# Optimization experiments

Hardware: AMD Instinct MI355X
Metric: run time of the kernel (lower is better)

Reference implementation:

```python
import jax, jax.numpy as jnp
import numpy as np

D_MODEL = 1024
N_HEAD = 16
D_HEAD = D_MODEL // N_HEAD


def setup_inputs() -> dict:
    key = jax.random.key(0)
    ks = jax.random.split(key, 6)
    B, T = 2, 2048
    scale = 1.0 / np.sqrt(D_MODEL)
    return {
        "x_q": jax.random.normal(ks[0], (B, T, D_MODEL), dtype=jnp.float32),
        "x_kv": jax.random.normal(ks[1], (B, T, D_MODEL), dtype=jnp.float32),
        "w_q": jax.random.normal(ks[2], (D_MODEL, D_MODEL), dtype=jnp.float32) * scale,
        "w_k": jax.random.normal(ks[3], (D_MODEL, D_MODEL), dtype=jnp.float32) * scale,
        "w_v": jax.random.normal(ks[4], (D_MODEL, D_MODEL), dtype=jnp.float32) * scale,
        "w_o": jax.random.normal(ks[5], (D_MODEL, D_MODEL), dtype=jnp.float32) * scale,
    }


def reference(x_q, x_kv, w_q, w_k, w_v, w_o):
    B, Tq, C = x_q.shape
    Tk = x_kv.shape[1]
    # torch Linear: y = x @ W.T  (W is [out, in])
    q = (x_q @ w_q.T).reshape(B, Tq, N_HEAD, D_HEAD).transpose(0, 2, 1, 3)
    k = (x_kv @ w_k.T).reshape(B, Tk, N_HEAD, D_HEAD).transpose(0, 2, 1, 3)
    v = (x_kv @ w_v.T).reshape(B, Tk, N_HEAD, D_HEAD).transpose(0, 2, 1, 3)
    scores = jnp.einsum('bhqd,bhkd->bhqk', q, k) / jnp.sqrt(jnp.float32(D_HEAD))
    attn = jax.nn.softmax(scores, axis=-1)  # [B, H, Tq, Tk]
    out = jnp.einsum('bhqk,bhkd->bhqd', attn, v)
    out = out.transpose(0, 2, 1, 3).reshape(B, Tq, C)
    out = out @ w_o.T
    return (out, attn)
```

## Files before the change

### kernel.cpp

```cpp
#include <hip/hip_runtime.h>
#include <stdint.h>
#include <type_traits>

typedef unsigned short u16;
typedef __attribute__((ext_vector_type(8))) short bf16x8;
typedef __attribute__((ext_vector_type(4))) float f32x4;
typedef __attribute__((ext_vector_type(4))) int   i32x4;

#define TSEQ   2048
#define DMODEL 1024
#define NHEAD  16
#define DHEAD  64
#define SCALE2 0.18033688011112042f

__device__ __forceinline__ u16 f2bf(float f) {
  union { float f; uint32_t u; } v; v.f = f;
  uint32_t r = v.u + 0x7FFFu + ((v.u >> 16) & 1u);
  return (u16)(r >> 16);
}

__device__ __forceinline__ float bf2f(uint32_t bits) {
  union { uint32_t u; float f; } v; v.u = bits << 16;
  return v.f;
}

__device__ __forceinline__ void ldsbar() {
  asm volatile("s_waitcnt lgkmcnt(0)\ns_barrier" ::: "memory");
}

__device__ __forceinline__ void gload16(const u16* src, u16* dst) {
  __builtin_amdgcn_global_load_lds(
      (const __attribute__((address_space(1))) void*)src,
      (__attribute__((address_space(3))) void*)dst, 16, 0, 0);
}

__global__ void cvt_all(const float* __restrict__ x_q, const float* __restrict__ x_kv,
                        const float* __restrict__ w_q, const float* __restrict__ w_k,
                        const float* __restrict__ w_v, const float* __restrict__ w_o,
                        u16* __restrict__ dst) {
  int i = blockIdx.x * blockDim.x + threadIdx.x;
  const float4* src;
  if (i < (1 << 20)) {
    src = (const float4*)x_q + i;
  } else if (i < (2 << 20)) {
    src = (const float4*)x_kv + (i - (1 << 20));
  } else {
    int r = i - (2 << 20);
    int k = r >> 18;
    int off = r & ((1 << 18) - 1);
    const float* w = (k == 0) ? w_q : (k == 1) ? w_k : (k == 2) ? w_v : w_o;
    src = (const float4*)w + off;
  }
  float4 f = *src;
  ushort4 o;
  o.x = f2bf(f.x); o.y = f2bf(f.y); o.z = f2bf(f.z); o.w = f2bf(f.w);
  ((ushort4*)dst)[i] = o;
}

template <typename OUT_T, bool TRANSZ2, int BM>
__global__ __launch_bounds__(256, 3)
void gemm_bt(const u16* A0, const u16* W0, void* C0,
             const u16* A1, const u16* W1, void* C1,
             const u16* A2, const u16* W2, void* C2,
             int M, int N, int K) {
  const u16* A = A0; const u16* W = W0; void* Cv = C0;
  if (blockIdx.z == 1) { A = A1; W = W1; Cv = C1; }
  if (blockIdx.z == 2) { A = A2; W = W2; Cv = C2; }

  constexpr int MW = BM / 32;
  constexpr int STG = BM * 64 + 128 * 64;
  constexpr int LSZ = (STG > 16896) ? STG : 16896;
  __shared__ u16 lS[LSZ];
  u16* lA = lS;
  u16* lB = lS + BM * 64;

  const int tid  = threadIdx.x;
  const int lane = tid & 63;
  const int wid  = tid >> 6;
  const int wr = wid >> 1, wc = wid & 1;
  const int g = lane >> 4, l15 = lane & 15;
  const int row0 = blockIdx.y * BM;
  const int col0 = blockIdx.x * 128;
  const int lrow = lane >> 3;
  const int lcol = (lane & 7) * 8;

  const f32x4 vz = {0.f, 0.f, 0.f, 0.f};
  f32x4 acc[MW][4];
#pragma unroll
  for (int m = 0; m < MW; ++m)
#pragma unroll
    for (int n = 0; n < 4; ++n) acc[m][n] = vz;

  for (int k0 = 0; k0 < K; k0 += 64) {
    __syncthreads();
#pragma unroll
    for (int i = 0; i < BM / 32; ++i) {
      int r = wid * (BM / 4) + i * 8;
      gload16(&A[(size_t)(row0 + r + lrow) * K + k0 + lcol], &lA[r * 64]);
    }
#pragma unroll
    for (int i = 0; i < 4; ++i) {
      int r = wid * 32 + i * 8;
      gload16(&W[(size_t)(col0 + r + lrow) * K + k0 + lcol], &lB[r * 64]);
    }
    __syncthreads();
#pragma unroll
    for (int kk = 0; kk < 2; ++kk) {
      bf16x8 af[MW], bfr[4];
#pragma unroll
      for (int m = 0; m < MW; ++m)
        af[m] = *(const bf16x8*)&lA[(wr * (BM / 2) + m * 16 + l15) * 64 + kk * 32 + g * 8];
#pragma unroll
      for (int n = 0; n < 4; ++n)
        bfr[n] = *(const bf16x8*)&lB[(wc * 64 + n * 16 + l15) * 64 + kk * 32 + g * 8];
#pragma unroll
      for (int m = 0; m < MW; ++m)
#pragma unroll
        for (int n = 0; n < 4; ++n)
          acc[m][n] = __builtin_amdgcn_mfma_f32_16x16x32_bf16(af[m], bfr[n], acc[m][n], 0, 0, 0);
    }
  }

  __syncthreads();

  if constexpr (TRANSZ2) {
    if (blockIdx.z == 2) {
      u16* lC = lS;
#pragma unroll
      for (int m = 0; m < MW; ++m)
#pragma unroll
        for (int n = 0; n < 4; ++n) {
          const int c  = wc * 64 + n * 16 + l15;
          const int r0 = wr * (BM / 2) + m * 16 + g * 4;
          uint64_t pk = (uint64_t)f2bf(acc[m][n][0]) |
                        ((uint64_t)f2bf(acc[m][n][1]) << 16) |
                        ((uint64_t)f2bf(acc[m][n][2]) << 32) |
                        ((uint64_t)f2bf(acc[m][n][3]) << 48);
          *(uint64_t*)&lC[c * 132 + r0] = pk;
        }
      __syncthreads();
      u16* C = (u16*)Cv;
      const int bb  = row0 >> 11;
      const int t0b = row0 & 2047;
#pragma unroll
      for (int i = 0; i < (128 * BM) / (8 * 256); ++i) {
        int idx = i * 256 + tid;
        int cr  = idx >> (BM == 128 ? 4 : 3);
        int cc  = idx & ((BM == 128 ? 16 : 8) - 1);
        int ch  = col0 + cr;
        u16* dst = &C[(((size_t)(bb * NHEAD + (ch >> 6)) * DHEAD + (ch & 63)) * TSEQ) + t0b + cc * 8];
        *(i32x4*)dst = *(const i32x4*)&lC[cr * 132 + cc * 8];
      }
      return;
    }
  }
  if constexpr (std::is_same_v<OUT_T, u16>) {
    u16* lC = lS;
#pragma unroll
    for (int m = 0; m < MW; ++m)
#pragma unroll
      for (int n = 0; n < 4; ++n) {
        const int r = wr * (BM / 2) + m * 16 + g * 4;
        const int c = wc * 64 + n * 16 + l15;
#pragma unroll
        for (int j = 0; j < 4; ++j) lC[(r + j) * 132 + c] = f2bf(acc[m][n][j]);
      }
    __syncthreads();
    u16* C = (u16*)Cv;
#pragma unroll
    for (int i = 0; i < (BM * 128) / (8 * 256); ++i) {
      int idx = i * 256 + tid;
      int r  = idx >> 4;
      int cc = idx & 15;
      *(i32x4*)&C[(size_t)(row0 + r) * N + col0 + cc * 8] =
          *(const i32x4*)&lC[r * 132 + cc * 8];
    }
  } else {
    float* lC = (float*)lS;
#pragma unroll
    for (int m = 0; m < MW; ++m)
#pragma unroll
      for (int n = 0; n < 4; ++n) {
        const int r = wr * (BM / 2) + m * 16 + g * 4;
        const int c = wc * 64 + n * 16 + l15;
#pragma unroll
        for (int j = 0; j < 4; ++j) lC[(r + j) * 132 + c] = acc[m][n][j];
      }
    __syncthreads();
    float* C = (float*)Cv;
#pragma unroll
    for (int i = 0; i < (BM * 128) / (4 * 256); ++i) {
      int idx = i * 256 + tid;
      int r  = idx >> 5;
      int cc = idx & 31;
      *(f32x4*)&C[(size_t)(row0 + r) * N + col0 + cc * 4] =
          *(const f32x4*)&lC[r * 132 + cc * 4];
    }
  }
}

__global__ __launch_bounds__(256, 2)
void attn_fused(const u16* __restrict__ Qb, const u16* __restrict__ Kb,
                const u16* __restrict__ VTb, float* __restrict__ attn,
                u16* __restrict__ Ob) {
  __shared__ u16 lP[2][128 * 136];
  __shared__ float lL[2][128];
  __shared__ float lInv[128];

  const int tid  = threadIdx.x;
  const int lane = tid & 63;
  const int wid  = tid >> 6;
  const int wq = wid & 1, wt = wid >> 1;
  const int g = lane >> 4, l15 = lane & 15;

  const int flat = blockIdx.x + 16 * blockIdx.y;
  const int xcd  = flat & 7;
  const int idx  = flat >> 3;
  const int bh   = xcd + 8 * (idx >> 4);
  const int q0   = (idx & 15) * 128;
  const int b    = bh >> 4;

  const size_t xbase  = (size_t)b * TSEQ * DMODEL + (size_t)(bh & 15) * DHEAD;
  const size_t vtbase = (size_t)bh * DHEAD * TSEQ;

  bf16x8 qf[4][2];
#pragma unroll
  for (int n = 0; n < 4; ++n)
#pragma unroll
    for (int kk = 0; kk < 2; ++kk)
      qf[n][kk] = *(const bf16x8*)&Qb[xbase + (size_t)(q0 + wq * 64 + n * 16 + l15) * DMODEL + kk * 32 + g * 8];

  const f32x4 vz = {0.f, 0.f, 0.f, 0.f};
  float psum[4] = {0.f, 0.f, 0.f, 0.f};

  const u16* kbase = Kb + xbase + (size_t)(wt * 64 + l15) * DMODEL + g * 8;

  for (int t0 = 0; t0 < TSEQ; t0 += 128) {
    f32x4 s[4][4];
#pragma unroll
    for (int m = 0; m < 4; ++m)
#pragma unroll
      for (int n = 0; n < 4; ++n) s[m][n] = vz;
#pragma unroll
    for (int kk = 0; kk < 2; ++kk) {
      bf16x8 kf[4];
#pragma unroll
      for (int m = 0; m < 4; ++m)
        kf[m] = *(const bf16x8*)&kbase[(size_t)(t0 + m * 16) * DMODEL + kk * 32];
#pragma unroll
      for (int m = 0; m < 4; ++m)
#pragma unroll
        for (int n = 0; n < 4; ++n)
          s[m][n] = __builtin_amdgcn_mfma_f32_16x16x32_bf16(kf[m], qf[n][kk], s[m][n], 0, 0, 0);
    }
#pragma unroll
    for (int m = 0; m < 4; ++m)
#pragma unroll
      for (int n = 0; n < 4; ++n)
#pragma unroll
        for (int j = 0; j < 4; ++j)
          psum[n] += __builtin_amdgcn_exp2f(s[m][n][j] * SCALE2);
  }

#pragma unroll
  for (int n = 0; n < 4; ++n) {
    psum[n] += __shfl_xor(psum[n], 16);
    psum[n] += __shfl_xor(psum[n], 32);
  }
  if (lane < 16) {
#pragma unroll
    for (int n = 0; n < 4; ++n) lL[wt][wq * 64 + n * 16 + lane] = psum[n];
  }
  __syncthreads();
  if (tid < 128) lInv[tid] = 1.0f / (lL[0][tid] + lL[1][tid]);
  __syncthreads();

  float inv_c[16];
#pragma unroll
  for (int c = 0; c < 16; ++c) inv_c[c] = lInv[c * 8 + (tid >> 5)];

  f32x4 accO[2][4];
#pragma unroll
  for (int mi = 0; mi < 2; ++mi)
#pragma unroll
    for (int ni = 0; ni < 4; ++ni) accO[mi][ni] = vz;

  const u16* vbase = VTb + vtbase + (size_t)l15 * TSEQ + g * 8;
  float* attn_tb = attn + ((size_t)bh * TSEQ + q0) * TSEQ;

  int cur = 0;
  for (int t0 = 0; t0 < TSEQ; t0 += 128) {
    u16* lPc = lP[cur];

    {
      f32x4 s[4][4];
#pragma unroll
      for (int m = 0; m < 4; ++m)
#pragma unroll
        for (int n = 0; n < 4; ++n) s[m][n] = vz;
#pragma unroll
      for (int kk = 0; kk < 2; ++kk) {
        bf16x8 kf[4];
#pragma unroll
        for (int m = 0; m < 4; ++m)
          kf[m] = *(const bf16x8*)&kbase[(size_t)(t0 + m * 16) * DMODEL + kk * 32];
#pragma unroll
        for (int m = 0; m < 4; ++m)
#pragma unroll
          for (int n = 0; n < 4; ++n)
            s[m][n] = __builtin_amdgcn_mfma_f32_16x16x32_bf16(kf[m], qf[n][kk], s[m][n], 0, 0, 0);
      }

#pragma unroll
      for (int m = 0; m < 4; ++m)
#pragma unroll
        for (int n = 0; n < 4; ++n) {
          const int q  = wq * 64 + n * 16 + l15;
          const int tt = wt * 64 + m * 16 + g * 4;
          u16 pb[4];
#pragma unroll
          for (int j = 0; j < 4; ++j)
            pb[j] = f2bf(__builtin_amdgcn_exp2f(s[m][n][j] * SCALE2));
          uint64_t pkk = (uint64_t)pb[0] | ((uint64_t)pb[1] << 16) |
                         ((uint64_t)pb[2] << 32) | ((uint64_t)pb[3] << 48);
          *(uint64_t*)&lPc[q * 136 + tt] = pkk;
        }
    }
    ldsbar();

    bf16x8 vf[4][4];
#pragma unroll
    for (int kt = 0; kt < 4; ++kt)
#pragma unroll
      for (int ni = 0; ni < 4; ++ni)
        vf[kt][ni] = *(const bf16x8*)&vbase[(size_t)(ni * 16) * TSEQ + t0 + kt * 32];

#pragma unroll
    for (int c = 0; c < 16; ++c) {
      const int fl = c * 1024 + tid * 4;
      const int q  = fl >> 7;
      const int t  = fl & 127;
      uint64_t pkv = *(const uint64_t*)&lPc[q * 136 + t];
      const float inv = inv_c[c];
      f32x4 pv;
#pragma unroll
      for (int j = 0; j < 4; ++j)
        pv[j] = bf2f((uint32_t)(pkv >> (16 * j)) & 0xFFFFu) * inv;
      __builtin_nontemporal_store(pv, (f32x4*)&attn_tb[(size_t)q * TSEQ + t0 + t]);
    }

#pragma unroll
    for (int kt = 0; kt < 4; ++kt) {
      bf16x8 pf[2];
#pragma unroll
      for (int mi = 0; mi < 2; ++mi)
        pf[mi] = *(const bf16x8*)&lPc[(wid * 32 + mi * 16 + l15) * 136 + kt * 32 + g * 8];
#pragma unroll
      for (int mi = 0; mi < 2; ++mi)
#pragma unroll
        for (int ni = 0; ni < 4; ++ni)
          accO[mi][ni] = __builtin_amdgcn_mfma_f32_16x16x32_bf16(pf[mi], vf[kt][ni], accO[mi][ni], 0, 0, 0);
    }
    cur ^= 1;
  }

#pragma unroll
  for (int mi = 0; mi < 2; ++mi)
#pragma unroll
    for (int ni = 0; ni < 4; ++ni)
#pragma unroll
      for (int j = 0; j < 4; ++j) {
        int q = wid * 32 + mi * 16 + g * 4 + j;
        Ob[xbase + (size_t)(q0 + q) * DMODEL + ni * 16 + l15] = f2bf(accO[mi][ni][j] * lInv[q]);
      }
}

extern "C" void kernel_launch(void* const* d_in, const int* in_sizes, int n_in,
                              void* d_out, int out_size, void* d_ws, size_t ws_size,
                              hipStream_t stream) {
  const float* x_q  = (const float*)d_in[0];
  const float* x_kv = (const float*)d_in[1];
  const float* w_q  = (const float*)d_in[2];
  const float* w_k  = (const float*)d_in[3];
  const float* w_v  = (const float*)d_in[4];
  const float* w_o  = (const float*)d_in[5];

  float* out  = (float*)d_out;
  float* attn = out + (size_t)2 * TSEQ * DMODEL;

  const size_t X_E = (size_t)2 * TSEQ * DMODEL;
  const size_t W_E = (size_t)DMODEL * DMODEL;

  u16* ws     = (u16*)d_ws;
  u16* xq_bf  = ws;
  u16* xkv_bf = xq_bf + X_E;
  u16* wq_bf  = xkv_bf + X_E;
  u16* wk_bf  = wq_bf + W_E;
  u16* wv_bf  = wk_bf + W_E;
  u16* wo_bf  = wv_bf + W_E;
  u16* q_bf   = wo_bf + W_E;
  u16* k_bf   = q_bf + X_E;
  u16* vt_bf  = k_bf + X_E;
  u16* o_bf   = vt_bf + X_E;

  cvt_all<<<dim3(3 * 1024 * 1024 / 256), dim3(256), 0, stream>>>(
      x_q, x_kv, w_q, w_k, w_v, w_o, ws);

  {
    dim3 grid(DMODEL / 128, (2 * TSEQ) / 128, 3);
    gemm_bt<u16, true, 128><<<grid, dim3(256), 0, stream>>>(
        xq_bf,  wq_bf, q_bf,
        xkv_bf, wk_bf, k_bf,
        xkv_bf, wv_bf, vt_bf,
        2 * TSEQ, DMODEL, DMODEL);
  }

  attn_fused<<<dim3(TSEQ / 128, 2 * NHEAD), dim3(256), 0, stream>>>(
      q_bf, k_bf, vt_bf, attn, o_bf);

  {
    dim3 grid(DMODEL / 128, (2 * TSEQ) / 64, 1);
    gemm_bt<float, false, 64><<<grid, dim3(256), 0, stream>>>(
        o_bf, wo_bf, out,
        o_bf, wo_bf, out,
        o_bf, wo_bf, out,
        2 * TSEQ, DMODEL, DMODEL);
  }
}
```

Before: 230.2 us.

## Cache full 16-row score strip in LDS to avoid recomputing QK^T

Shrinks the attention query tile from 128 to 16 rows and stores the whole 16x2048 bf16 exp-score strip in LDS during the first pass. The second pass no longer recomputes QK^T; it reads probabilities from LDS for the normalized attn write and the PV MMA. This removes the duplicated score GEMM and exp work, but K and V^T are now re-read from global/L2 for every 16-row tile, which is 8x more blocks touching K/V. The large LDS footprint (~66KB) may also limit occupancy.

```diff
diff --git a/kernel.cpp b/kernel.cpp
--- a/kernel.cpp
+++ b/kernel.cpp
@@ -12,6 +12,8 @@
 #define NHEAD  16
 #define DHEAD  64
 #define SCALE2 0.18033688011112042f
+#define QT     16
+#define SPITCH 2056
 
 __device__ __forceinline__ u16 f2bf(float f) {
   union { float f; uint32_t u; } v; v.f = f;
@@ -22,10 +24,6 @@
 __device__ __forceinline__ float bf2f(uint32_t bits) {
   union { uint32_t u; float f; } v; v.u = bits << 16;
   return v.f;
-}
-
-__device__ __forceinline__ void ldsbar() {
-  asm volatile("s_waitcnt lgkmcnt(0)\ns_barrier" ::: "memory");
 }
 
 __device__ __forceinline__ void gload16(const u16* src, u16* dst) {
@@ -203,176 +201,107 @@
 void attn_fused(const u16* __restrict__ Qb, const u16* __restrict__ Kb,
                 const u16* __restrict__ VTb, float* __restrict__ attn,
                 u16* __restrict__ Ob) {
-  __shared__ u16 lP[2][128 * 136];
-  __shared__ float lL[2][128];
-  __shared__ float lInv[128];
+  __shared__ u16  lS[QT * SPITCH];
+  __shared__ float lL[4][16];
+  __shared__ float lInv[16];
 
   const int tid  = threadIdx.x;
   const int lane = tid & 63;
   const int wid  = tid >> 6;
-  const int wq = wid & 1, wt = wid >> 1;
   const int g = lane >> 4, l15 = lane & 15;
 
-  const int flat = blockIdx.x + 16 * blockIdx.y;
+  const int flat = blockIdx.x + 128 * blockIdx.y;
   const int xcd  = flat & 7;
   const int idx  = flat >> 3;
-  const int bh   = xcd + 8 * (idx >> 4);
-  const int q0   = (idx & 15) * 128;
+  const int bh   = xcd + 8 * (idx >> 7);
+  const int q0   = (idx & 127) * QT;
   const int b    = bh >> 4;
 
   const size_t xbase  = (size_t)b * TSEQ * DMODEL + (size_t)(bh & 15) * DHEAD;
   const size_t vtbase = (size_t)bh * DHEAD * TSEQ;
 
-  bf16x8 qf[4][2];
-#pragma unroll
-  for (int n = 0; n < 4; ++n)
-#pragma unroll
-    for (int kk = 0; kk < 2; ++kk)
-      qf[n][kk] = *(const bf16x8*)&Qb[xbase + (size_t)(q0 + wq * 64 + n * 16 + l15) * DMODEL + kk * 32 + g * 8];
+  bf16x8 qf[2];
+#pragma unroll
+  for (int kk = 0; kk < 2; ++kk)
+    qf[kk] = *(const bf16x8*)&Qb[xbase + (size_t)(q0 + l15) * DMODEL + kk * 32 + g * 8];
 
   const f32x4 vz = {0.f, 0.f, 0.f, 0.f};
-  float psum[4] = {0.f, 0.f, 0.f, 0.f};
-
-  const u16* kbase = Kb + xbase + (size_t)(wt * 64 + l15) * DMODEL + g * 8;
+  float psum = 0.f;
+
+  const u16* kbase = Kb + xbase + (size_t)(wid * 32 + l15) * DMODEL + g * 8;
 
   for (int t0 = 0; t0 < TSEQ; t0 += 128) {
-    f32x4 s[4][4];
-#pragma unroll
-    for (int m = 0; m < 4; ++m)
-#pragma unroll
-      for (int n = 0; n < 4; ++n) s[m][n] = vz;
+    f32x4 s[2];
+    s[0] = vz; s[1] = vz;
 #pragma unroll
     for (int kk = 0; kk < 2; ++kk) {
-      bf16x8 kf[4];
-#pragma unroll
-      for (int m = 0; m < 4; ++m)
+      bf16x8 kf[2];
+#pragma unroll
+      for (int m = 0; m < 2; ++m)
         kf[m] = *(const bf16x8*)&kbase[(size_t)(t0 + m * 16) * DMODEL + kk * 32];
 #pragma unroll
-      for (int m = 0; m < 4; ++m)
-#pragma unroll
-        for (int n = 0; n < 4; ++n)
-          s[m][n] = __builtin_amdgcn_mfma_f32_16x16x32_bf16(kf[m], qf[n][kk], s[m][n], 0, 0, 0);
-    }
-#pragma unroll
-    for (int m = 0; m < 4; ++m)
-#pragma unroll
-      for (int n = 0; n < 4; ++n)
-#pragma unroll
-        for (int j = 0; j < 4; ++j)
-          psum[n] += __builtin_amdgcn_exp2f(s[m][n][j] * SCALE2);
-  }
-
-#pragma unroll
-  for (int n = 0; n < 4; ++n) {
-    psum[n] += __shfl_xor(psum[n], 16);
-    psum[n] += __shfl_xor(psum[n], 32);
-  }
-  if (lane < 16) {
-#pragma unroll
-    for (int n = 0; n < 4; ++n) lL[wt][wq * 64 + n * 16 + lane] = psum[n];
-  }
+      for (int m = 0; m < 2; ++m)
+        s[m] = __builtin_amdgcn_mfma_f32_16x16x32_bf16(kf[m], qf[kk], s[m], 0, 0, 0);
+    }
+#pragma unroll
+    for (int m = 0; m < 2; ++m) {
+      u16 pb[4];
+#pragma unroll
+      for (int j = 0; j < 4; ++j) {
+        float p = __builtin_amdgcn_exp2f(s[m][j] * SCALE2);
+        psum += p;
+        pb[j] = f2bf(p);
+      }
+      const int tt = t0 + wid * 32 + m * 16 + g * 4;
+      uint64_t pkk = (uint64_t)pb[0] | ((uint64_t)pb[1] << 16) |
+                     ((uint64_t)pb[2] << 32) | ((uint64_t)pb[3] << 48);
+      *(uint64_t*)&lS[l15 * SPITCH + tt] = pkk;
+    }
+  }
+
+  psum += __shfl_xor(psum, 16);
+  psum += __shfl_xor(psum, 32);
+  if (lane < 16) lL[wid][lane] = psum;
   __syncthreads();
-  if (tid < 128) lInv[tid] = 1.0f / (lL[0][tid] + lL[1][tid]);
+  if (tid < 16) lInv[tid] = 1.0f / (lL[0][tid] + lL[1][tid] + lL[2][tid] + lL[3][tid]);
   __syncthreads();
 
-  float inv_c[16];
-#pragma unroll
-  for (int c = 0; c < 16; ++c) inv_c[c] = lInv[c * 8 + (tid >> 5)];
-
-  f32x4 accO[2][4];
-#pragma unroll
-  for (int mi = 0; mi < 2; ++mi)
-#pragma unroll
-    for (int ni = 0; ni < 4; ++ni) accO[mi][ni] = vz;
-
-  const u16* vbase = VTb + vtbase + (size_t)l15 * TSEQ + g * 8;
+  float inv_r[2];
+  inv_r[0] = lInv[tid >> 5];
+  inv_r[1] = lInv[8 + (tid >> 5)];
+  float inv_j[4];
+#pragma unroll
+  for (int j = 0; j < 4; ++j) inv_j[j] = lInv[g * 4 + j];
+
+  f32x4 accO = vz;
+  const u16* vbase = VTb + vtbase + (size_t)(wid * 16 + l15) * TSEQ + g * 8;
   float* attn_tb = attn + ((size_t)bh * TSEQ + q0) * TSEQ;
 
-  int cur = 0;
   for (int t0 = 0; t0 < TSEQ; t0 += 128) {
-    u16* lPc = lP[cur];
-
-    {
-      f32x4 s[4][4];
-#pragma unroll
-      for (int m = 0; m < 4; ++m)
-#pragma unroll
-        for (int n = 0; n < 4; ++n) s[m][n] = vz;
-#pragma unroll
-      for (int kk = 0; kk < 2; ++kk) {
-        bf16x8 kf[4];
-#pragma unroll
-        for (int m = 0; m < 4; ++m)
-          kf[m] = *(const bf16x8*)&kbase[(size_t)(t0 + m * 16) * DMODEL + kk * 32];
-#pragma unroll
-        for (int m = 0; m < 4; ++m)
-#pragma unroll
-          for (int n = 0; n < 4; ++n)
-            s[m][n] = __builtin_amdgcn_mfma_f32_16x16x32_bf16(kf[m], qf[n][kk], s[m][n], 0, 0, 0);
-      }
-
-#pragma unroll
-      for (int m = 0; m < 4; ++m)
-#pragma unroll
-        for (int n = 0; n < 4; ++n) {
-          const int q  = wq * 64 + n * 16 + l15;
-          const int tt = wt * 64 + m * 16 + g * 4;
-          u16 pb[4];
-#pragma unroll
-          for (int j = 0; j < 4; ++j)
-            pb[j] = f2bf(__builtin_amdgcn_exp2f(s[m][n][j] * SCALE2));
-          uint64_t pkk = (uint64_t)pb[0] | ((uint64_t)pb[1] << 16) |
-                         ((uint64_t)pb[2] << 32) | ((uint64_t)pb[3] << 48);
-          *(uint64_t*)&lPc[q * 136 + tt] = pkk;
-        }
-    }
-    ldsbar();
-
-    bf16x8 vf[4][4];
-#pragma unroll
-    for (int kt = 0; kt < 4; ++kt)
-#pragma unroll
-      for (int ni = 0; ni < 4; ++ni)
-        vf[kt][ni] = *(const bf16x8*)&vbase[(size_t)(ni * 16) * TSEQ + t0 + kt * 32];
-
-#pragma unroll
-    for (int c = 0; c < 16; ++c) {
-      const int fl = c * 1024 + tid * 4;
-      const int q  = fl >> 7;
-      const int t  = fl & 127;
-      uint64_t pkv = *(const uint64_t*)&lPc[q * 136 + t];
-      const float inv = inv_c[c];
+#pragma unroll
+    for (int r = 0; r < 2; ++r) {
+      const int q  = r * 8 + (tid >> 5);
+      const int tq = (tid & 31) * 4;
+      uint64_t pkv = *(const uint64_t*)&lS[q * SPITCH + t0 + tq];
+      const float inv = inv_r[r];
       f32x4 pv;
 #pragma unroll
       for (int j = 0; j < 4; ++j)
         pv[j] = bf2f((uint32_t)(pkv >> (16 * j)) & 0xFFFFu) * inv;
-      __builtin_nontemporal_store(pv, (f32x4*)&attn_tb[(size_t)q * TSEQ + t0 + t]);
+      __builtin_nontemporal_store(pv, (f32x4*)&attn_tb[(size_t)q * TSEQ + t0 + tq]);
     }
 
 #pragma unroll
     for (int kt = 0; kt < 4; ++kt) {
-      bf16x8 pf[2];
-#pragma unroll
-      for (int mi = 0; mi < 2; ++mi)
-        pf[mi] = *(const bf16x8*)&lPc[(wid * 32 + mi * 16 + l15) * 136 + kt * 32 + g * 8];
-#pragma unroll
-      for (int mi = 0; mi < 2; ++mi)
-#pragma unroll
-        for (int ni = 0; ni < 4; ++ni)
-          accO[mi][ni] = __builtin_amdgcn_mfma_f32_16x16x32_bf16(pf[mi], vf[kt][ni], accO[mi][ni], 0, 0, 0);
-    }
-    cur ^= 1;
-  }
-
-#pragma unroll
-  for (int mi = 0; mi < 2; ++mi)
-#pragma unroll
-    for (int ni = 0; ni < 4; ++ni)
-#pragma unroll
-      for (int j = 0; j < 4; ++j) {
-        int q = wid * 32 + mi * 16 + g * 4 + j;
-        Ob[xbase + (size_t)(q0 + q) * DMODEL + ni * 16 + l15] = f2bf(accO[mi][ni][j] * lInv[q]);
-      }
+      bf16x8 pf = *(const bf16x8*)&lS[l15 * SPITCH + t0 + kt * 32 + g * 8];
+      bf16x8 vf = *(const bf16x8*)&vbase[t0 + kt * 32];
+      accO = __builtin_amdgcn_mfma_f32_16x16x32_bf16(pf, vf, accO, 0, 0, 0);
+    }
+  }
+
+#pragma unroll
+  for (int j = 0; j < 4; ++j)
+    Ob[xbase + (size_t)(q0 + g * 4 + j) * DMODEL + wid * 16 + l15] = f2bf(accO[j] * inv_j[j]);
 }
 
 extern "C" void kernel_launch(void* const* d_in, const int* in_sizes, int n_in,
@@ -415,7 +344,7 @@
         2 * TSEQ, DMODEL, DMODEL);
   }
 
-  attn_fused<<<dim3(TSEQ / 128, 2 * NHEAD), dim3(256), 0, stream>>>(
+  attn_fused<<<dim3(TSEQ / QT, 2 * NHEAD), dim3(256), 0, stream>>>(
       q_bf, k_bf, vt_bf, attn, o_bf);
 
   {
```

Measured after the change: 320.7 us. 1.39x slower.

## Split fused attention into separate row-sum stats and main attention kernels

Applied to the files above, without the earlier changes.

The single attention kernel, which first computed softmax row sums and then recomputed scores to write the attention matrix and output, is split into two launches. One computes inverse row sums into a global workspace and the other reads them back. This lets the stats pass run without the large double-buffered P shared-memory allocation, so it may get higher occupancy and lower register pressure. The cost is an extra launch, a small global round-trip for the statistics, and reloading the Q fragments in the second kernel.

```diff
diff --git a/kernel.cpp b/kernel.cpp
--- a/kernel.cpp
+++ b/kernel.cpp
@@ -200,12 +200,9 @@
 }
 
 __global__ __launch_bounds__(256, 2)
-void attn_fused(const u16* __restrict__ Qb, const u16* __restrict__ Kb,
-                const u16* __restrict__ VTb, float* __restrict__ attn,
-                u16* __restrict__ Ob) {
-  __shared__ u16 lP[2][128 * 136];
+void attn_stats(const u16* __restrict__ Qb, const u16* __restrict__ Kb,
+                float* __restrict__ invG) {
   __shared__ float lL[2][128];
-  __shared__ float lInv[128];
 
   const int tid  = threadIdx.x;
   const int lane = tid & 63;
@@ -220,8 +217,7 @@
   const int q0   = (idx & 15) * 128;
   const int b    = bh >> 4;
 
-  const size_t xbase  = (size_t)b * TSEQ * DMODEL + (size_t)(bh & 15) * DHEAD;
-  const size_t vtbase = (size_t)bh * DHEAD * TSEQ;
+  const size_t xbase = (size_t)b * TSEQ * DMODEL + (size_t)(bh & 15) * DHEAD;
 
   bf16x8 qf[4][2];
 #pragma unroll
@@ -232,7 +228,6 @@
 
   const f32x4 vz = {0.f, 0.f, 0.f, 0.f};
   float psum[4] = {0.f, 0.f, 0.f, 0.f};
-
   const u16* kbase = Kb + xbase + (size_t)(wt * 64 + l15) * DMODEL + g * 8;
 
   for (int t0 = 0; t0 < TSEQ; t0 += 128) {
@@ -272,12 +267,50 @@
     for (int n = 0; n < 4; ++n) lL[wt][wq * 64 + n * 16 + lane] = psum[n];
   }
   __syncthreads();
-  if (tid < 128) lInv[tid] = 1.0f / (lL[0][tid] + lL[1][tid]);
+  if (tid < 128)
+    invG[(size_t)bh * TSEQ + q0 + tid] = 1.0f / (lL[0][tid] + lL[1][tid]);
+}
+
+__global__ __launch_bounds__(256, 2)
+void attn_main(const u16* __restrict__ Qb, const u16* __restrict__ Kb,
+               const u16* __restrict__ VTb, const float* __restrict__ invG,
+               float* __restrict__ attn, u16* __restrict__ Ob) {
+  __shared__ u16 lP[2][128 * 136];
+  __shared__ float lInv[128];
+
+  const int tid  = threadIdx.x;
+  const int lane = tid & 63;
+  const int wid  = tid >> 6;
+  const int wq = wid & 1, wt = wid >> 1;
+  const int g = lane >> 4, l15 = lane & 15;
+
+  const int flat = blockIdx.x + 16 * blockIdx.y;
+  const int xcd  = flat & 7;
+  const int idx  = flat >> 3;
+  const int bh   = xcd + 8 * (idx >> 4);
+  const int q0   = (idx & 15) * 128;
+  const int b    = bh >> 4;
+
+  const size_t xbase  = (size_t)b * TSEQ * DMODEL + (size_t)(bh & 15) * DHEAD;
+  const size_t vtbase = (size_t)bh * DHEAD * TSEQ;
+
+  if (tid < 128) lInv[tid] = invG[(size_t)bh * TSEQ + q0 + tid];
+
+  bf16x8 qf[4][2];
+#pragma unroll
+  for (int n = 0; n < 4; ++n)
+#pragma unroll
+    for (int kk = 0; kk < 2; ++kk)
+      qf[n][kk] = *(const bf16x8*)&Qb[xbase + (size_t)(q0 + wq * 64 + n * 16 + l15) * DMODEL + kk * 32 + g * 8];
+
   __syncthreads();
 
   float inv_c[16];
 #pragma unroll
   for (int c = 0; c < 16; ++c) inv_c[c] = lInv[c * 8 + (tid >> 5)];
+
+  const f32x4 vz = {0.f, 0.f, 0.f, 0.f};
+  const u16* kbase = Kb + xbase + (size_t)(wt * 64 + l15) * DMODEL + g * 8;
 
   f32x4 accO[2][4];
 #pragma unroll
@@ -402,6 +435,7 @@
   u16* k_bf   = q_bf + X_E;
   u16* vt_bf  = k_bf + X_E;
   u16* o_bf   = vt_bf + X_E;
+  float* invG = (float*)(o_bf + X_E);
 
   cvt_all<<<dim3(3 * 1024 * 1024 / 256), dim3(256), 0, stream>>>(
       x_q, x_kv, w_q, w_k, w_v, w_o, ws);
@@ -415,8 +449,10 @@
         2 * TSEQ, DMODEL, DMODEL);
   }
 
-  attn_fused<<<dim3(TSEQ / 128, 2 * NHEAD), dim3(256), 0, stream>>>(
-      q_bf, k_bf, vt_bf, attn, o_bf);
+  attn_stats<<<dim3(TSEQ / 128, 2 * NHEAD), dim3(256), 0, stream>>>(
+      q_bf, k_bf, invG);
+  attn_main<<<dim3(TSEQ / 128, 2 * NHEAD), dim3(256), 0, stream>>>(
+      q_bf, k_bf, vt_bf, invG, attn, o_bf);
 
   {
     dim3 grid(DMODEL / 128, (2 * TSEQ) / 64, 1);
```

New measurement: 239.1 us. 1.04x slower.
